# Optimization experiments

Measured on AMD Instinct MI355X. Metric: run time of the kernel, lower is better.

The kernel has to match this reference:

```python
import jax, jax.numpy as jnp
import numpy as np

V, D = 50000, 300          # word vocab / embedding dim
P, M = 8, 512              # number of POS experts / candidates per expert
B, L, HS = 8, 1024, 512    # batch, seq len, ctx feature size (ctx_fs*2)
N_POS_TOTAL = 16           # POS alphabet size; experts cover ids 0..P-1
EPS = 1e-12


def setup_inputs() -> dict:
    key = jax.random.key(0)
    ks = jax.random.split(key, 8)
    inp_word = jax.random.randint(ks[0], (B, L), 0, V)
    inp_pos = jax.random.randint(ks[1], (B, L), 0, N_POS_TOTAL)
    ctx = jax.random.normal(ks[2], (B, L, HS), dtype=jnp.float32)
    word_emb_weight = jax.random.normal(ks[3], (V, D), dtype=jnp.float32)
    dec_W = jax.random.normal(ks[4], (P, HS, M), dtype=jnp.float32) * (1.0 / np.sqrt(HS))
    dec_b = jax.random.normal(ks[5], (P, M), dtype=jnp.float32) * 0.01
    tgt_words = jax.random.randint(ks[6], (P, M), 0, V)
    u = jax.random.uniform(ks[7], (P, B * L, M), dtype=jnp.float32, minval=1e-8, maxval=1.0 - 1e-8)
    gumbel = -jnp.log(-jnp.log(u))  # standard Gumbel(0,1) noise
    return {"inp_word": inp_word, "inp_pos": inp_pos, "ctx": ctx,
            "word_emb_weight": word_emb_weight, "dec_W": dec_W, "dec_b": dec_b,
            "tgt_words": tgt_words, "gumbel": gumbel}


def reference(inp_word, inp_pos, ctx, word_emb_weight, dec_W, dec_b, tgt_words, gumbel):
    t = 1.0  # eval-mode temperature (get_temperature only in training)
    T = B * L
    ctx2 = ctx.reshape(T, HS)
    word_flat = inp_word.reshape(T)
    pos_flat = inp_pos.reshape(T)

    # per-POS expert decode: Linear + Softmax, then log(p + eps)   [P, T, M]
    logits = jnp.einsum('td,pdm->ptm', ctx2, dec_W) + dec_b[:, None, :]
    pspt = jnp.log(jax.nn.softmax(logits, axis=-1) + EPS)
    # gumbel-softmax sample
    sft = jax.nn.softmax((pspt + gumbel) / t, axis=-1)            # [P, T, M]
    y = jnp.argmax(sft, axis=-1)                                  # [P, T]
    y_word = jnp.take_along_axis(tgt_words, y, axis=1)            # map wid -> word id, [P, T]
    tgt_emb = word_emb_weight[tgt_words]                          # [P, M, D]
    x_emb = jnp.einsum('ptm,pmd->ptd', sft, tgt_emb)              # [P, T, D]

    # masked scatter back by POS routing
    sel = (pos_flat[None, :] == jnp.arange(P, dtype=pos_flat.dtype)[:, None])  # [P, T]
    msk = pos_flat < P                                            # union of expert masks
    nn_msk = pos_flat < 2                                         # POS ids 0,1 play the 'NN*' role

    word_new = jnp.sum(jnp.where(sel, y_word, 0), axis=0)
    emb_new = jnp.einsum('pt,ptd->td', sel.astype(x_emb.dtype), x_emb)

    obf_word = jnp.where(msk, word_new, word_flat).reshape(B, L)
    base_emb = word_emb_weight[word_flat]
    obf_word_emb = jnp.where(msk[:, None], emb_new, base_emb).reshape(B, L, D)
    obf_mask = msk.astype(jnp.float32).reshape(B, L)
    nn_mask = nn_msk.reshape(B, L)
    return obf_word, obf_word_emb, obf_mask, nn_mask
```

## Files before the change

kernel.cpp:

```cpp
#include <hip/hip_runtime.h>
#include <cstddef>

#define T_TOT 8192
#define M_    512
#define HS_   512
#define D_    300
#define P_    8
#define TT    8
#define KSTEP 8
#define NSTEP (HS_ / KSTEP)
#define CNT_STRIDE 16

__device__ __forceinline__ void gload_lds16(const float* g, float* l) {
    __builtin_amdgcn_global_load_lds(
        (const __attribute__((address_space(1))) unsigned int*)g,
        (__attribute__((address_space(3))) unsigned int*)l, 16, 0, 0);
}

__global__ __launch_bounds__(256) void route_kernel(
    const int* __restrict__ inp_word, const int* __restrict__ inp_pos,
    int* __restrict__ cnt, int* __restrict__ perm,
    float* __restrict__ out_word, float* __restrict__ out_maskm,
    float* __restrict__ out_maskn)
{
    __shared__ int lcnt[P_];
    __shared__ int lbase[P_];
    int tid = threadIdx.x;
    int t = blockIdx.x * 256 + tid;
    if (tid < P_) lcnt[tid] = 0;
    __syncthreads();

    int pp = inp_pos[t];
    out_maskm[t] = (pp < P_) ? 1.0f : 0.0f;
    out_maskn[t] = (pp < 2)  ? 1.0f : 0.0f;
    int loc = 0;
    if (pp < P_) {
        loc = atomicAdd(&lcnt[pp], 1);
    } else {
        out_word[t] = (float)inp_word[t];
    }
    __syncthreads();
    if (tid < P_) lbase[tid] = atomicAdd(&cnt[tid * CNT_STRIDE], lcnt[tid]);
    __syncthreads();
    if (pp < P_) perm[pp * T_TOT + lbase[pp] + loc] = t;
}

__global__ __launch_bounds__(128) void base_emb_kernel(
    const int* __restrict__ inp_word, const int* __restrict__ inp_pos,
    const float* __restrict__ wemb, float* __restrict__ out_emb)
{
    int t = blockIdx.x;
    if (inp_pos[t] < P_) return;
    int w = inp_word[t];
    if (threadIdx.x < 75) {
        float4 v = *(const float4*)&wemb[(size_t)w * D_ + threadIdx.x * 4];
        *(float4*)&out_emb[(size_t)t * D_ + threadIdx.x * 4] = v;
    }
}

__global__ __launch_bounds__(256, 3) void expert_kernel(
    const float* __restrict__ ctx,   const float* __restrict__ wemb,
    const float* __restrict__ dec_W, const float* __restrict__ dec_b,
    const int*   __restrict__ tgt,   const float* __restrict__ gumbel,
    const int*   __restrict__ cnt,   const int*   __restrict__ perm,
    float* __restrict__ out_word,    float* __restrict__ out_emb)
{
    int p = blockIdx.x;
    int count = cnt[p * CNT_STRIDE];
    int start = blockIdx.y * TT;
    if (start >= count) return;
    int n = min(TT, count - start);

    __shared__ float ctxb[TT][HS_];
    __shared__ float wbuf[2][KSTEP][M_];
    __shared__ int   tok_ids[TT];
    __shared__ int   tw_s[M_];

    int tn = threadIdx.x;
    if (tn < TT) tok_ids[tn] = (tn < n) ? perm[p * T_TOT + start + tn] : -1;
    tw_s[tn]       = tgt[p * M_ + tn];
    tw_s[tn + 256] = tgt[p * M_ + tn + 256];
    __syncthreads();

    const float* Wp = dec_W + (size_t)p * HS_ * M_;

    #pragma unroll
    for (int r = 0; r < 4; ++r)
        gload_lds16(Wp + r * 1024 + tn * 4, &wbuf[0][0][0] + r * 1024 + tn * 4);

    #pragma unroll
    for (int it = 0; it < 4; ++it) {
        int idx  = tn + it * 256;
        int tok  = idx >> 7;
        int pos4 = idx & 127;
        int t = tok_ids[tok];
        float4 v = make_float4(0.f, 0.f, 0.f, 0.f);
        if (t >= 0) v = *(const float4*)&ctx[(size_t)t * HS_ + pos4 * 4];
        *(float4*)&ctxb[tok][pos4 * 4] = v;
    }
    __syncthreads();

    int m0 = tn * 2;
    float accA[TT], accB[TT];
    #pragma unroll
    for (int k = 0; k < TT; ++k) { accA[k] = 0.f; accB[k] = 0.f; }

    int cur = 0;
    for (int step = 0; step < NSTEP; ++step) {
        if (step + 1 < NSTEP) {
            const float* src = Wp + (size_t)(step + 1) * KSTEP * M_;
            float* dst = &wbuf[cur ^ 1][0][0];
            #pragma unroll
            for (int r = 0; r < 4; ++r)
                gload_lds16(src + r * 1024 + tn * 4, dst + r * 1024 + tn * 4);
        }
        #pragma unroll
        for (int h4 = 0; h4 < KSTEP / 4; ++h4) {
            float2 w0 = *(const float2*)&wbuf[cur][h4 * 4 + 0][m0];
            float2 w1 = *(const float2*)&wbuf[cur][h4 * 4 + 1][m0];
            float2 w2 = *(const float2*)&wbuf[cur][h4 * 4 + 2][m0];
            float2 w3 = *(const float2*)&wbuf[cur][h4 * 4 + 3][m0];
            #pragma unroll
            for (int k = 0; k < TT; ++k) {
                float4 c = *(const float4*)&ctxb[k][step * KSTEP + h4 * 4];
                accA[k] = fmaf(c.x, w0.x, fmaf(c.y, w1.x, fmaf(c.z, w2.x, fmaf(c.w, w3.x, accA[k]))));
                accB[k] = fmaf(c.x, w0.y, fmaf(c.y, w1.y, fmaf(c.z, w2.y, fmaf(c.w, w3.y, accB[k]))));
            }
        }
        __syncthreads();
        cur ^= 1;
    }

    float b0 = dec_b[p * M_ + m0];
    float b1 = dec_b[p * M_ + m0 + 1];
    #pragma unroll
    for (int k = 0; k < TT; ++k) {
        *(float2*)&ctxb[k][m0] = make_float2(accA[k] + b0, accB[k] + b1);
    }
    __syncthreads();

    int wave = tn >> 6, lane = tn & 63;
    for (int tok = wave * 2; tok < wave * 2 + 2; ++tok) {
        if (tok >= n) continue;
        int t = tok_ids[tok];
        float l[8];
        #pragma unroll
        for (int j = 0; j < 8; ++j) l[j] = ctxb[tok][j * 64 + lane];
        float mx = l[0];
        #pragma unroll
        for (int j = 1; j < 8; ++j) mx = fmaxf(mx, l[j]);
        for (int off = 32; off; off >>= 1) mx = fmaxf(mx, __shfl_xor(mx, off, 64));

        float ex[8];
        float se = 0.f;
        #pragma unroll
        for (int j = 0; j < 8; ++j) { ex[j] = expf(l[j] - mx); se += ex[j]; }
        for (int off = 32; off; off >>= 1) se += __shfl_xor(se, off, 64);

        const float* gp = gumbel + ((size_t)p * T_TOT + t) * M_;
        float s[8];
        float bm = -3.0e38f;
        int   bi = 0x7fffffff;
        #pragma unroll
        for (int j = 0; j < 8; ++j) {
            float q  = ex[j] / se;
            float sv = logf(q + 1e-12f) + gp[j * 64 + lane];
            s[j] = sv;
            if (sv > bm) { bm = sv; bi = j * 64 + lane; }
        }
        for (int off = 32; off; off >>= 1) {
            float ov = __shfl_xor(bm, off, 64);
            int   oi = __shfl_xor(bi, off, 64);
            if (ov > bm || (ov == bm && oi < bi)) { bm = ov; bi = oi; }
        }

        float e2[8];
        float s2 = 0.f;
        #pragma unroll
        for (int j = 0; j < 8; ++j) { e2[j] = expf(s[j] - bm); s2 += e2[j]; }
        for (int off = 32; off; off >>= 1) s2 += __shfl_xor(s2, off, 64);

        #pragma unroll
        for (int j = 0; j < 8; ++j) ctxb[tok][j * 64 + lane] = e2[j] / s2;

        if (lane == 0) out_word[t] = (float)tw_s[bi];
    }
    __syncthreads();

    if (tn < 150) {
        int d0 = tn * 2;
        float acA[TT], acB[TT];
        #pragma unroll
        for (int k = 0; k < TT; ++k) { acA[k] = 0.f; acB[k] = 0.f; }

        #pragma unroll 2
        for (int m4 = 0; m4 < M_ / 4; ++m4) {
            int t0 = tw_s[m4 * 4 + 0];
            int t1 = tw_s[m4 * 4 + 1];
            int t2 = tw_s[m4 * 4 + 2];
            int t3 = tw_s[m4 * 4 + 3];
            float2 e0  = *(const float2*)&wemb[(size_t)t0 * D_ + d0];
            float2 e1  = *(const float2*)&wemb[(size_t)t1 * D_ + d0];
            float2 e2v = *(const float2*)&wemb[(size_t)t2 * D_ + d0];
            float2 e3  = *(const float2*)&wemb[(size_t)t3 * D_ + d0];
            #pragma unroll
            for (int k = 0; k < TT; ++k) {
                float4 sv = *(const float4*)&ctxb[k][m4 * 4];
                acA[k] = fmaf(sv.x, e0.x, fmaf(sv.y, e1.x, fmaf(sv.z, e2v.x, fmaf(sv.w, e3.x, acA[k]))));
                acB[k] = fmaf(sv.x, e0.y, fmaf(sv.y, e1.y, fmaf(sv.z, e2v.y, fmaf(sv.w, e3.y, acB[k]))));
            }
        }
        #pragma unroll
        for (int k = 0; k < TT; ++k) {
            if (k < n) {
                int t = tok_ids[k];
                *(float2*)&out_emb[(size_t)t * D_ + d0] = make_float2(acA[k], acB[k]);
            }
        }
    }
}

extern "C" void kernel_launch(void* const* d_in, const int* in_sizes, int n_in,
                              void* d_out, int out_size, void* d_ws, size_t ws_size,
                              hipStream_t stream)
{
    const int*   inp_word = (const int*)d_in[0];
    const int*   inp_pos  = (const int*)d_in[1];
    const float* ctx      = (const float*)d_in[2];
    const float* wemb     = (const float*)d_in[3];
    const float* dec_W    = (const float*)d_in[4];
    const float* dec_b    = (const float*)d_in[5];
    const int*   tgt      = (const int*)d_in[6];
    const float* gumbel   = (const float*)d_in[7];

    float* out       = (float*)d_out;
    float* out_word  = out;
    float* out_emb   = out + T_TOT;
    float* out_maskm = out + T_TOT + T_TOT * D_;
    float* out_maskn = out_maskm + T_TOT;

    int* cnt  = (int*)d_ws;
    int* perm = cnt + P_ * CNT_STRIDE;

    hipMemsetAsync(d_ws, 0, P_ * CNT_STRIDE * sizeof(int), stream);
    route_kernel<<<T_TOT / 256, 256, 0, stream>>>(
        inp_word, inp_pos, cnt, perm, out_word, out_maskm, out_maskn);
    base_emb_kernel<<<T_TOT, 128, 0, stream>>>(inp_word, inp_pos, wemb, out_emb);
    expert_kernel<<<dim3(P_, T_TOT / TT), 256, 0, stream>>>(
        ctx, wemb, dec_W, dec_b, tgt, gumbel, cnt, perm, out_word, out_emb);
}
```

Baseline: 340.3 us.

## Use persistent 512-thread expert blocks processing 16-token chunks

Expert kernel now launches a fixed grid of 32 blocks per expert with 512 threads, looping over 16-token chunks instead of launching one 8-token block per chunk with many early exits. Two halves of the block each compute 8 tokens of the decoder GEMM sharing the same streamed weight tiles, halving dec_W and embedding-table traffic per token. The embedding projection now uses one output column per thread across 300 threads. Fewer blocks may reduce latency hiding and parallelism if token counts are uneven.

```diff
diff --git a/kernel.cpp b/kernel.cpp
--- a/kernel.cpp
+++ b/kernel.cpp
@@ -6,7 +6,8 @@
 #define HS_   512
 #define D_    300
 #define P_    8
-#define TT    8
+#define TT    16
+#define NBLK_Y 32
 #define KSTEP 8
 #define NSTEP (HS_ / KSTEP)
 #define CNT_STRIDE 16
@@ -58,7 +59,7 @@
     }
 }
 
-__global__ __launch_bounds__(256, 3) void expert_kernel(
+__global__ __launch_bounds__(512, 2) void expert_kernel(
     const float* __restrict__ ctx,   const float* __restrict__ wemb,
     const float* __restrict__ dec_W, const float* __restrict__ dec_b,
     const int*   __restrict__ tgt,   const float* __restrict__ gumbel,
@@ -67,9 +68,6 @@
 {
     int p = blockIdx.x;
     int count = cnt[p * CNT_STRIDE];
-    int start = blockIdx.y * TT;
-    if (start >= count) return;
-    int n = min(TT, count - start);
 
     __shared__ float ctxb[TT][HS_];
     __shared__ float wbuf[2][KSTEP][M_];
@@ -77,146 +75,154 @@
     __shared__ int   tw_s[M_];
 
     int tn = threadIdx.x;
-    if (tn < TT) tok_ids[tn] = (tn < n) ? perm[p * T_TOT + start + tn] : -1;
-    tw_s[tn]       = tgt[p * M_ + tn];
-    tw_s[tn + 256] = tgt[p * M_ + tn + 256];
-    __syncthreads();
+    tw_s[tn] = tgt[p * M_ + tn];
 
     const float* Wp = dec_W + (size_t)p * HS_ * M_;
-
-    #pragma unroll
-    for (int r = 0; r < 4; ++r)
-        gload_lds16(Wp + r * 1024 + tn * 4, &wbuf[0][0][0] + r * 1024 + tn * 4);
-
-    #pragma unroll
-    for (int it = 0; it < 4; ++it) {
-        int idx  = tn + it * 256;
-        int tok  = idx >> 7;
-        int pos4 = idx & 127;
-        int t = tok_ids[tok];
-        float4 v = make_float4(0.f, 0.f, 0.f, 0.f);
-        if (t >= 0) v = *(const float4*)&ctx[(size_t)t * HS_ + pos4 * 4];
-        *(float4*)&ctxb[tok][pos4 * 4] = v;
-    }
-    __syncthreads();
-
-    int m0 = tn * 2;
-    float accA[TT], accB[TT];
-    #pragma unroll
-    for (int k = 0; k < TT; ++k) { accA[k] = 0.f; accB[k] = 0.f; }
-
-    int cur = 0;
-    for (int step = 0; step < NSTEP; ++step) {
-        if (step + 1 < NSTEP) {
-            const float* src = Wp + (size_t)(step + 1) * KSTEP * M_;
-            float* dst = &wbuf[cur ^ 1][0][0];
-            #pragma unroll
-            for (int r = 0; r < 4; ++r)
-                gload_lds16(src + r * 1024 + tn * 4, dst + r * 1024 + tn * 4);
-        }
-        #pragma unroll
-        for (int h4 = 0; h4 < KSTEP / 4; ++h4) {
-            float2 w0 = *(const float2*)&wbuf[cur][h4 * 4 + 0][m0];
-            float2 w1 = *(const float2*)&wbuf[cur][h4 * 4 + 1][m0];
-            float2 w2 = *(const float2*)&wbuf[cur][h4 * 4 + 2][m0];
-            float2 w3 = *(const float2*)&wbuf[cur][h4 * 4 + 3][m0];
-            #pragma unroll
-            for (int k = 0; k < TT; ++k) {
-                float4 c = *(const float4*)&ctxb[k][step * KSTEP + h4 * 4];
-                accA[k] = fmaf(c.x, w0.x, fmaf(c.y, w1.x, fmaf(c.z, w2.x, fmaf(c.w, w3.x, accA[k]))));
-                accB[k] = fmaf(c.x, w0.y, fmaf(c.y, w1.y, fmaf(c.z, w2.y, fmaf(c.w, w3.y, accB[k]))));
-            }
-        }
-        __syncthreads();
-        cur ^= 1;
-    }
-
+    int tl = tn & 255;
+    int half = tn >> 8;
+    int m0 = tl * 2;
+    int tokbase = half * 8;
     float b0 = dec_b[p * M_ + m0];
     float b1 = dec_b[p * M_ + m0 + 1];
-    #pragma unroll
-    for (int k = 0; k < TT; ++k) {
-        *(float2*)&ctxb[k][m0] = make_float2(accA[k] + b0, accB[k] + b1);
-    }
-    __syncthreads();
-
     int wave = tn >> 6, lane = tn & 63;
-    for (int tok = wave * 2; tok < wave * 2 + 2; ++tok) {
-        if (tok >= n) continue;
-        int t = tok_ids[tok];
-        float l[8];
-        #pragma unroll
-        for (int j = 0; j < 8; ++j) l[j] = ctxb[tok][j * 64 + lane];
-        float mx = l[0];
-        #pragma unroll
-        for (int j = 1; j < 8; ++j) mx = fmaxf(mx, l[j]);
-        for (int off = 32; off; off >>= 1) mx = fmaxf(mx, __shfl_xor(mx, off, 64));
-
-        float ex[8];
-        float se = 0.f;
-        #pragma unroll
-        for (int j = 0; j < 8; ++j) { ex[j] = expf(l[j] - mx); se += ex[j]; }
-        for (int off = 32; off; off >>= 1) se += __shfl_xor(se, off, 64);
-
-        const float* gp = gumbel + ((size_t)p * T_TOT + t) * M_;
-        float s[8];
-        float bm = -3.0e38f;
-        int   bi = 0x7fffffff;
-        #pragma unroll
-        for (int j = 0; j < 8; ++j) {
-            float q  = ex[j] / se;
-            float sv = logf(q + 1e-12f) + gp[j * 64 + lane];
-            s[j] = sv;
-            if (sv > bm) { bm = sv; bi = j * 64 + lane; }
-        }
-        for (int off = 32; off; off >>= 1) {
-            float ov = __shfl_xor(bm, off, 64);
-            int   oi = __shfl_xor(bi, off, 64);
-            if (ov > bm || (ov == bm && oi < bi)) { bm = ov; bi = oi; }
-        }
-
-        float e2[8];
-        float s2 = 0.f;
-        #pragma unroll
-        for (int j = 0; j < 8; ++j) { e2[j] = expf(s[j] - bm); s2 += e2[j]; }
-        for (int off = 32; off; off >>= 1) s2 += __shfl_xor(s2, off, 64);
-
-        #pragma unroll
-        for (int j = 0; j < 8; ++j) ctxb[tok][j * 64 + lane] = e2[j] / s2;
-
-        if (lane == 0) out_word[t] = (float)tw_s[bi];
-    }
-    __syncthreads();
-
-    if (tn < 150) {
-        int d0 = tn * 2;
-        float acA[TT], acB[TT];
-        #pragma unroll
-        for (int k = 0; k < TT; ++k) { acA[k] = 0.f; acB[k] = 0.f; }
-
-        #pragma unroll 2
-        for (int m4 = 0; m4 < M_ / 4; ++m4) {
-            int t0 = tw_s[m4 * 4 + 0];
-            int t1 = tw_s[m4 * 4 + 1];
-            int t2 = tw_s[m4 * 4 + 2];
-            int t3 = tw_s[m4 * 4 + 3];
-            float2 e0  = *(const float2*)&wemb[(size_t)t0 * D_ + d0];
-            float2 e1  = *(const float2*)&wemb[(size_t)t1 * D_ + d0];
-            float2 e2v = *(const float2*)&wemb[(size_t)t2 * D_ + d0];
-            float2 e3  = *(const float2*)&wemb[(size_t)t3 * D_ + d0];
+
+    for (int chunk = blockIdx.y; chunk * TT < count; chunk += NBLK_Y) {
+        int start = chunk * TT;
+        int n = min(TT, count - start);
+
+        if (tn < TT) tok_ids[tn] = (tn < n) ? perm[p * T_TOT + start + tn] : -1;
+        __syncthreads();
+
+        gload_lds16(Wp + tn * 4,        &wbuf[0][0][0] + tn * 4);
+        gload_lds16(Wp + 2048 + tn * 4, &wbuf[0][0][0] + 2048 + tn * 4);
+
+        #pragma unroll
+        for (int it = 0; it < 4; ++it) {
+            int idx  = tn + it * 512;
+            int tok  = idx >> 7;
+            int pos4 = idx & 127;
+            int t = tok_ids[tok];
+            float4 v = make_float4(0.f, 0.f, 0.f, 0.f);
+            if (t >= 0) v = *(const float4*)&ctx[(size_t)t * HS_ + pos4 * 4];
+            *(float4*)&ctxb[tok][pos4 * 4] = v;
+        }
+        __syncthreads();
+
+        float accA[8], accB[8];
+        #pragma unroll
+        for (int k = 0; k < 8; ++k) { accA[k] = 0.f; accB[k] = 0.f; }
+
+        int cur = 0;
+        for (int step = 0; step < NSTEP; ++step) {
+            if (step + 1 < NSTEP) {
+                const float* src = Wp + (size_t)(step + 1) * KSTEP * M_;
+                float* dst = &wbuf[cur ^ 1][0][0];
+                gload_lds16(src + tn * 4,        dst + tn * 4);
+                gload_lds16(src + 2048 + tn * 4, dst + 2048 + tn * 4);
+            }
+            #pragma unroll
+            for (int h4 = 0; h4 < KSTEP / 4; ++h4) {
+                float2 w0 = *(const float2*)&wbuf[cur][h4 * 4 + 0][m0];
+                float2 w1 = *(const float2*)&wbuf[cur][h4 * 4 + 1][m0];
+                float2 w2 = *(const float2*)&wbuf[cur][h4 * 4 + 2][m0];
+                float2 w3 = *(const float2*)&wbuf[cur][h4 * 4 + 3][m0];
+                #pragma unroll
+                for (int k = 0; k < 8; ++k) {
+                    float4 c = *(const float4*)&ctxb[tokbase + k][step * KSTEP + h4 * 4];
+                    accA[k] = fmaf(c.x, w0.x, fmaf(c.y, w1.x, fmaf(c.z, w2.x, fmaf(c.w, w3.x, accA[k]))));
+                    accB[k] = fmaf(c.x, w0.y, fmaf(c.y, w1.y, fmaf(c.z, w2.y, fmaf(c.w, w3.y, accB[k]))));
+                }
+            }
+            __syncthreads();
+            cur ^= 1;
+        }
+
+        #pragma unroll
+        for (int k = 0; k < 8; ++k) {
+            *(float2*)&ctxb[tokbase + k][m0] = make_float2(accA[k] + b0, accB[k] + b1);
+        }
+        __syncthreads();
+
+        #pragma unroll
+        for (int ti = 0; ti < 2; ++ti) {
+            int tok = wave * 2 + ti;
+            if (tok >= n) continue;
+            int t = tok_ids[tok];
+            float l[8];
+            #pragma unroll
+            for (int j = 0; j < 8; ++j) l[j] = ctxb[tok][j * 64 + lane];
+            float mx = l[0];
+            #pragma unroll
+            for (int j = 1; j < 8; ++j) mx = fmaxf(mx, l[j]);
+            for (int off = 32; off; off >>= 1) mx = fmaxf(mx, __shfl_xor(mx, off, 64));
+
+            float ex[8];
+            float se = 0.f;
+            #pragma unroll
+            for (int j = 0; j < 8; ++j) { ex[j] = expf(l[j] - mx); se += ex[j]; }
+            for (int off = 32; off; off >>= 1) se += __shfl_xor(se, off, 64);
+
+            const float* gp = gumbel + ((size_t)p * T_TOT + t) * M_;
+            float s[8];
+            float bm = -3.0e38f;
+            int   bi = 0x7fffffff;
+            #pragma unroll
+            for (int j = 0; j < 8; ++j) {
+                float q  = ex[j] / se;
+                float sv = logf(q + 1e-12f) + gp[j * 64 + lane];
+                s[j] = sv;
+                if (sv > bm) { bm = sv; bi = j * 64 + lane; }
+            }
+            for (int off = 32; off; off >>= 1) {
+                float ov = __shfl_xor(bm, off, 64);
+                int   oi = __shfl_xor(bi, off, 64);
+                if (ov > bm || (ov == bm && oi < bi)) { bm = ov; bi = oi; }
+            }
+
+            float e2[8];
+            float s2 = 0.f;
+            #pragma unroll
+            for (int j = 0; j < 8; ++j) { e2[j] = expf(s[j] - bm); s2 += e2[j]; }
+            for (int off = 32; off; off >>= 1) s2 += __shfl_xor(s2, off, 64);
+
+            #pragma unroll
+            for (int j = 0; j < 8; ++j) ctxb[tok][j * 64 + lane] = e2[j] / s2;
+
+            if (lane == 0) out_word[t] = (float)tw_s[bi];
+        }
+        __syncthreads();
+
+        if (tn < D_) {
+            int d0 = tn;
+            float ac[TT];
+            #pragma unroll
+            for (int k = 0; k < TT; ++k) ac[k] = 0.f;
+
+            #pragma unroll 4
+            for (int m4 = 0; m4 < M_ / 4; ++m4) {
+                int t0 = tw_s[m4 * 4 + 0];
+                int t1 = tw_s[m4 * 4 + 1];
+                int t2 = tw_s[m4 * 4 + 2];
+                int t3 = tw_s[m4 * 4 + 3];
+                float e0 = wemb[(size_t)t0 * D_ + d0];
+                float e1 = wemb[(size_t)t1 * D_ + d0];
+                float e2 = wemb[(size_t)t2 * D_ + d0];
+                float e3 = wemb[(size_t)t3 * D_ + d0];
+                #pragma unroll
+                for (int k = 0; k < TT; ++k) {
+                    float4 sv = *(const float4*)&ctxb[k][m4 * 4];
+                    ac[k] = fmaf(sv.x, e0, fmaf(sv.y, e1, fmaf(sv.z, e2, fmaf(sv.w, e3, ac[k]))));
+                }
+            }
             #pragma unroll
             for (int k = 0; k < TT; ++k) {
-                float4 sv = *(const float4*)&ctxb[k][m4 * 4];
-                acA[k] = fmaf(sv.x, e0.x, fmaf(sv.y, e1.x, fmaf(sv.z, e2v.x, fmaf(sv.w, e3.x, acA[k]))));
-                acB[k] = fmaf(sv.x, e0.y, fmaf(sv.y, e1.y, fmaf(sv.z, e2v.y, fmaf(sv.w, e3.y, acB[k]))));
-            }
-        }
-        #pragma unroll
-        for (int k = 0; k < TT; ++k) {
-            if (k < n) {
-                int t = tok_ids[k];
-                *(float2*)&out_emb[(size_t)t * D_ + d0] = make_float2(acA[k], acB[k]);
-            }
-        }
+                if (k < n) {
+                    int t = tok_ids[k];
+                    out_emb[(size_t)t * D_ + d0] = ac[k];
+                }
+            }
+        }
+        __syncthreads();
     }
 }
 
@@ -246,6 +252,6 @@
     route_kernel<<<T_TOT / 256, 256, 0, stream>>>(
         inp_word, inp_pos, cnt, perm, out_word, out_maskm, out_maskn);
     base_emb_kernel<<<T_TOT, 128, 0, stream>>>(inp_word, inp_pos, wemb, out_emb);
-    expert_kernel<<<dim3(P_, T_TOT / TT), 256, 0, stream>>>(
+    expert_kernel<<<dim3(P_, NBLK_Y), 512, 0, stream>>>(
         ctx, wemb, dec_W, dec_b, tgt, gumbel, cnt, perm, out_word, out_emb);
 }
```

Result: slower. 521.8 us (+53.4%).
